# Performance work log

Hardware: AMD Instinct MI355X
Metric: run time of the kernel (lower is better)

## Reference

```python
import jax, jax.numpy as jnp
import numpy as np

N0, N1, N2 = 400000, 75000, 15000
E1, E2 = 1200000, 240000
F_IN, NC = 64, 40
H1, C1 = 2, 8          # layer 1: heads=2, out_channels=8 -> concat dim 16
H2, C2 = 1, NC         # layer 2: heads=1, out_channels=num_classes
NEG_SLOPE = 0.2


def gat_conv(x_src, x_dst, src, dst, Ws, Wd, att_s, att_d, bias, heads, ch):
    """PyG GATConv on bipartite (x_src, x_dst) with remove+add self loops."""
    n_dst = x_dst.shape[0]
    hs = (x_src @ Ws).reshape(-1, heads, ch)   # [N_src, H, C]
    hd = (x_dst @ Wd).reshape(-1, heads, ch)   # [N_dst, H, C]
    a_s = (hs * att_s).sum(-1)                 # [N_src, H]
    a_d = (hd * att_d).sum(-1)                 # [N_dst, H]
    loops = jnp.arange(n_dst)
    src_all = jnp.concatenate([src, loops])
    dst_all = jnp.concatenate([dst, loops])
    # remove_self_loops: drop pre-existing i->i edges; add_self_loops: appended
    valid = jnp.concatenate([src != dst, jnp.ones(n_dst, dtype=bool)])[:, None]
    logits = jax.nn.leaky_relu(a_s[src_all] + a_d[dst_all], NEG_SLOPE)  # [E, H]
    logits = jnp.where(valid, logits, -jnp.inf)
    m = jax.ops.segment_max(logits, dst_all, num_segments=n_dst)        # [N_dst, H]
    w = jnp.where(valid, jnp.exp(logits - m[dst_all]), 0.0)
    denom = jax.ops.segment_sum(w, dst_all, num_segments=n_dst)
    alpha = w / denom[dst_all]                                          # [E, H]
    out = jax.ops.segment_sum(alpha[:, :, None] * hs[src_all], dst_all,
                              num_segments=n_dst)                       # [N_dst, H, C]
    return out.reshape(n_dst, heads * ch) + bias


def setup_inputs() -> dict:
    key = jax.random.key(0)
    ks = jax.random.split(key, 16)
    s = 0.1
    return {
        "x": jax.random.normal(ks[0], (N0, F_IN), dtype=jnp.float32),
        "e1_src": jax.random.randint(ks[1], (E1,), 0, N0),
        "e1_dst": jax.random.randint(ks[2], (E1,), 0, N1),
        "e2_src": jax.random.randint(ks[3], (E2,), 0, N1),
        "e2_dst": jax.random.randint(ks[4], (E2,), 0, N2),
        "W1s": jax.random.normal(ks[5], (F_IN, H1 * C1), dtype=jnp.float32) * s,
        "W1d": jax.random.normal(ks[6], (F_IN, H1 * C1), dtype=jnp.float32) * s,
        "att1_s": jax.random.normal(ks[7], (H1, C1), dtype=jnp.float32) * s,
        "att1_d": jax.random.normal(ks[8], (H1, C1), dtype=jnp.float32) * s,
        "b1": jnp.zeros((H1 * C1,), dtype=jnp.float32),
        "W2s": jax.random.normal(ks[9], (H1 * C1, H2 * C2), dtype=jnp.float32) * s,
        "W2d": jax.random.normal(ks[10], (H1 * C1, H2 * C2), dtype=jnp.float32) * s,
        "att2_s": jax.random.normal(ks[11], (H2, C2), dtype=jnp.float32) * s,
        "att2_d": jax.random.normal(ks[12], (H2, C2), dtype=jnp.float32) * s,
        "b2": jnp.zeros((H2 * C2,), dtype=jnp.float32),
    }


def reference(x, e1_src, e1_dst, e2_src, e2_dst,
              W1s, W1d, att1_s, att1_d, b1,
              W2s, W2d, att2_s, att2_d, b2):
    h = gat_conv(x, x[:N1], e1_src, e1_dst, W1s, W1d, att1_s, att1_d, b1, H1, C1)
    h = jax.nn.elu(h)
    o = gat_conv(h, h[:N2], e2_src, e2_dst, W2s, W2d, att2_s, att2_d, b2, H2, C2)
    return jax.nn.log_softmax(o, axis=-1)
```

## Files before the change

kernel.cpp:

```cpp
#include <hip/hip_runtime.h>
#include <hip/hip_bf16.h>

constexpr int N0 = 400000, N1 = 75000, N2 = 15000;
constexpr int E1 = 1200000, E2 = 240000;
constexpr int NC = 40;
constexpr float NEG_SLOPE = 0.2f;

constexpr int BK1 = 128;
constexpr int NB1 = (N1 + BK1 - 1) / BK1;
constexpr int CAPB1 = 2432;
constexpr int BK2 = 32;
constexpr int NB2 = (N2 + BK2 - 1) / BK2;
constexpr int CAPB2 = 704;

constexpr int TILE = 8192;
constexpr int NT1 = (E1 + TILE - 1) / TILE;
constexpr int NT2 = (E2 + TILE - 1) / TILE;
constexpr int BPJ = (N0 + 255) / 256;

using f32x4 = __attribute__((ext_vector_type(4))) float;
using s16x8 = __attribute__((ext_vector_type(8))) short;

__device__ __forceinline__ float leaky(float v) { return v > 0.f ? v : NEG_SLOPE * v; }

__device__ __forceinline__ unsigned cvtpk(float lo, float hi) {
    unsigned r;
    asm("v_cvt_pk_bf16_f32 %0, %1, %2" : "=v"(r) : "v"(lo), "v"(hi));
    return r;
}

__device__ __forceinline__ unsigned bf16pair(float lo, float hi) {
    unsigned a = __float_as_uint(lo), b = __float_as_uint(hi);
    a = (a + 0x7FFFu + ((a >> 16) & 1u)) >> 16;
    b = (b + 0x7FFFu + ((b >> 16) & 1u)) & 0xFFFF0000u;
    return a | b;
}
__device__ __forceinline__ float bfLo(unsigned w) { return __uint_as_float(w << 16); }
__device__ __forceinline__ float bfHi(unsigned w) { return __uint_as_float(w & 0xFFFF0000u); }

__global__ __launch_bounds__(256) void k1_kernel(
    const float* __restrict__ x,
    const float* __restrict__ W1s, const float* __restrict__ W1d,
    const float* __restrict__ att1s, const float* __restrict__ att1d,
    const int* __restrict__ e1s, const int* __restrict__ e1d,
    const int* __restrict__ e2s, const int* __restrict__ e2d,
    unsigned* __restrict__ rec1, float* __restrict__ a_d1,
    int* __restrict__ gcnt1, unsigned* __restrict__ bin1,
    int* __restrict__ gcnt2, unsigned* __restrict__ bin2)
{
    __shared__ int hist[NB1];
    __shared__ int gbase[NB1];

    int bid = blockIdx.x;
    const int tid = threadIdx.x;
    if (bid < NT1 + NT2) {
        const bool isL1 = bid < NT1;
        const int* es = isL1 ? e1s : e2s;
        const int* ed = isL1 ? e1d : e2d;
        const int nE = isL1 ? E1 : E2;
        const int nb = isL1 ? NB1 : NB2;
        const int cap = isL1 ? CAPB1 : CAPB2;
        const int shift = isL1 ? 7 : 5;
        const int lsh = isL1 ? 19 : 17;
        int* gc = isL1 ? gcnt1 : gcnt2;
        unsigned* gbin = isL1 ? bin1 : bin2;
        const int base = (isL1 ? bid : bid - NT1) * TILE;
        const int lim = min(TILE, nE - base);

        for (int b = tid; b < nb; b += 256) hist[b] = 0;
        __syncthreads();
        for (int i = tid; i < lim; i += 256) {
            int s = es[base + i], d = ed[base + i];
            if (s != d) atomicAdd(&hist[d >> shift], 1);
        }
        __syncthreads();
        for (int b = tid; b < nb; b += 256) {
            int c = hist[b];
            gbase[b] = (c > 0) ? atomicAdd(&gc[b], c) : 0;
            hist[b] = 0;
        }
        __syncthreads();
        for (int i = tid; i < lim; i += 256) {
            int s = es[base + i], d = ed[base + i];
            if (s != d) {
                int b = d >> shift;
                int pos = gbase[b] + atomicAdd(&hist[b], 1);
                if (pos < cap)
                    gbin[(size_t)b * cap + pos] =
                        (unsigned)s | ((unsigned)(d & ((1 << shift) - 1)) << lsh);
            }
        }
        return;
    }
    bid -= NT1 + NT2;
    const int l    = tid & 63;
    const int nd   = l & 15;
    const int kg   = l >> 4;
    const int wv   = tid >> 6;
    const int nodeBase = bid * 256;

    s16x8 bf0, bf1;
    {
        union { unsigned u[4]; s16x8 v; } t0, t1;
        #pragma unroll
        for (int q = 0; q < 4; ++q) {
            t0.u[q] = cvtpk(W1s[(8 * kg + 2 * q) * 16 + nd],
                            W1s[(8 * kg + 2 * q + 1) * 16 + nd]);
            t1.u[q] = cvtpk(W1s[(32 + 8 * kg + 2 * q) * 16 + nd],
                            W1s[(32 + 8 * kg + 2 * q + 1) * 16 + nd]);
        }
        bf0 = t0.v; bf1 = t1.v;
    }
    float att4[4];
    #pragma unroll
    for (int r = 0; r < 4; ++r) att4[r] = att1s[4 * kg + r];

    float vdh0[16], vdh1[16];
    if (nodeBase < N1) {
        #pragma unroll
        for (int m = 0; m < 2; ++m)
            #pragma unroll
            for (int j = 0; j < 8; ++j) {
                const float* wr = W1d + (size_t)(32 * m + 8 * kg + j) * 16;
                float d0 = 0.f, d1 = 0.f;
                #pragma unroll
                for (int cc = 0; cc < 8; ++cc) {
                    d0 = fmaf(wr[cc], att1d[cc], d0);
                    d1 = fmaf(wr[8 + cc], att1d[8 + cc], d1);
                }
                vdh0[m * 8 + j] = d0; vdh1[m * 8 + j] = d1;
            }
    }

    #pragma unroll 2
    for (int rnd = 0; rnd < 4; ++rnd) {
        const int base16 = nodeBase + rnd * 64 + wv * 16;
        if (base16 >= N0) break;
        const int node = base16 + nd;
        const float* xrow = x + (size_t)node * 64;
        float4 p0 = *(const float4*)(xrow + 8 * kg);
        float4 p1 = *(const float4*)(xrow + 8 * kg + 4);
        float4 p2 = *(const float4*)(xrow + 32 + 8 * kg);
        float4 p3 = *(const float4*)(xrow + 32 + 8 * kg + 4);

        union { unsigned u[4]; s16x8 v; } a0, a1;
        a0.u[0] = cvtpk(p0.x, p0.y); a0.u[1] = cvtpk(p0.z, p0.w);
        a0.u[2] = cvtpk(p1.x, p1.y); a0.u[3] = cvtpk(p1.z, p1.w);
        a1.u[0] = cvtpk(p2.x, p2.y); a1.u[1] = cvtpk(p2.z, p2.w);
        a1.u[2] = cvtpk(p3.x, p3.y); a1.u[3] = cvtpk(p3.z, p3.w);

        f32x4 acc = {0.f, 0.f, 0.f, 0.f};
        acc = __builtin_amdgcn_mfma_f32_16x16x32_bf16(bf0, a0.v, acc, 0, 0, 0);
        acc = __builtin_amdgcn_mfma_f32_16x16x32_bf16(bf1, a1.v, acc, 0, 0, 0);

        uint2 hw;
        hw.x = cvtpk(acc[0], acc[1]);
        hw.y = cvtpk(acc[2], acc[3]);
        unsigned* rp = rec1 + (size_t)node * 16;
        *(uint2*)(rp + 2 * kg) = hw;

        float p = acc[0] * att4[0];
        p = fmaf(acc[1], att4[1], p);
        p = fmaf(acc[2], att4[2], p);
        p = fmaf(acc[3], att4[3], p);
        p += __shfl_xor(p, 16, 64);
        float q = __shfl_xor(p, 32, 64);
        if (kg == 0)
            *(uint4*)(rp + 8) = make_uint4(__float_as_uint(p), __float_as_uint(q), 0u, 0u);
        else if (kg == 1)
            *(uint4*)(rp + 12) = make_uint4(0u, 0u, 0u, 0u);

        if (base16 < N1) {
            float xv8[16] = {p0.x, p0.y, p0.z, p0.w, p1.x, p1.y, p1.z, p1.w,
                             p2.x, p2.y, p2.z, p2.w, p3.x, p3.y, p3.z, p3.w};
            float d0 = 0.f, d1 = 0.f;
            #pragma unroll
            for (int j = 0; j < 16; ++j) {
                d0 = fmaf(xv8[j], vdh0[j], d0);
                d1 = fmaf(xv8[j], vdh1[j], d1);
            }
            d0 += __shfl_xor(d0, 16, 64); d0 += __shfl_xor(d0, 32, 64);
            d1 += __shfl_xor(d1, 16, 64); d1 += __shfl_xor(d1, 32, 64);
            if (kg == 0 && node < N1)
                ((float2*)a_d1)[node] = make_float2(d0, d1);
        }
    }
}

__global__ __launch_bounds__(512) void k2_kernel(
    const int* __restrict__ gcnt1, const unsigned* __restrict__ bin1,
    const unsigned* __restrict__ rec1, const float* __restrict__ a_d1,
    const float* __restrict__ b1,
    const float* __restrict__ W2s, const float* __restrict__ W2d,
    const float* __restrict__ att2s, const float* __restrict__ att2d,
    unsigned* __restrict__ rec2)
{
    __shared__ unsigned srt[CAPB1];
    __shared__ int hist[BK1], start[BK1 + 1];
    __shared__ float w2sl[640], va[16], vd[16];
    __shared__ float h1s[BK1][17];

    const int b = blockIdx.x, tid = threadIdx.x;
    const int d0 = b * BK1;
    const int nN = min(BK1, N1 - d0);
    const int ncnt = min(gcnt1[b], CAPB1);
    const unsigned* bp = bin1 + (size_t)b * CAPB1;

    for (int i = tid; i < 640; i += 512) w2sl[i] = W2s[i];
    if (tid < BK1) hist[tid] = 0;
    if (tid >= 128 && tid < 144) {
        int k = tid - 128;
        float sa = 0.f, sd = 0.f;
        for (int cc = 0; cc < 40; ++cc) {
            sa = fmaf(W2s[k * 40 + cc], att2s[cc], sa);
            sd = fmaf(W2d[k * 40 + cc], att2d[cc], sd);
        }
        va[k] = sa; vd[k] = sd;
    }
    __syncthreads();
    for (int i = tid; i < ncnt; i += 512) atomicAdd(&hist[bp[i] >> 19], 1);
    __syncthreads();
    if (tid == 0) {
        int a = 0;
        for (int k = 0; k < BK1; ++k) { start[k] = a; a += hist[k]; }
        start[BK1] = a;
    }
    __syncthreads();
    if (tid < BK1) hist[tid] = start[tid];
    __syncthreads();
    for (int i = tid; i < ncnt; i += 512) {
        unsigned p = bp[i];
        int pos = atomicAdd(&hist[p >> 19], 1);
        srt[pos] = p & 0x7FFFFu;
    }
    __syncthreads();

    const int g = tid >> 4, c = tid & 15, h = c >> 3;
    const int wbase = tid & 48;
    const int wmap = (c < 8) ? c : (8 + ((c >> 2) & 1));
    for (int n = g; n < nN; n += 32) {
        const int node = d0 + n;
        const float ad = a_d1[(size_t)node * 2 + h];
        const int st = start[n], cnt = start[n + 1] - start[n];
        unsigned rw0 = rec1[(size_t)node * 16 + wmap];
        unsigned rw1 = (cnt >= 1) ? rec1[(size_t)srt[st] * 16 + wmap] : 0u;
        unsigned rw2 = (cnt >= 2) ? rec1[(size_t)srt[st + 1] * 16 + wmap] : 0u;
        unsigned rw3 = (cnt >= 3) ? rec1[(size_t)srt[st + 2] * 16 + wmap] : 0u;
        float accv = 0.f, den = 0.f;
        for (int j = 0; j <= cnt; ++j) {
            float asv = __uint_as_float((unsigned)__shfl((int)rw0, wbase + 8 + 4 * h, 64));
            unsigned chw = (unsigned)__shfl((int)rw0, wbase + (c >> 1), 64);
            float hv = (c & 1) ? bfHi(chw) : bfLo(chw);
            float w = __expf(leaky(asv + ad));
            accv = fmaf(w, hv, accv);
            den += w;
            rw0 = rw1; rw1 = rw2; rw2 = rw3;
            rw3 = (j + 4 <= cnt) ? rec1[(size_t)srt[st + j + 3] * 16 + wmap] : 0u;
        }
        float v = accv / den + b1[c];
        h1s[n][c] = v > 0.f ? v : (__expf(v) - 1.f);
    }
    __syncthreads();
    for (int i = tid; i < nN * 24; i += 512) {
        int nn = i / 24, w = i - nn * 24;
        unsigned* rp = rec2 + (size_t)(d0 + nn) * 24;
        if (w < 20) {
            int c0 = 2 * w, c1 = c0 + 1;
            float s0 = 0.f, s1 = 0.f;
            #pragma unroll
            for (int k = 0; k < 16; ++k) {
                float hk = h1s[nn][k];
                s0 = fmaf(hk, w2sl[k * 40 + c0], s0);
                s1 = fmaf(hk, w2sl[k * 40 + c1], s1);
            }
            rp[w] = bf16pair(s0, s1);
        } else if (w < 22) {
            const float* vv = (w == 20) ? va : vd;
            float s = 0.f;
            #pragma unroll
            for (int k = 0; k < 16; ++k) s = fmaf(h1s[nn][k], vv[k], s);
            rp[w] = __float_as_uint(s);
        }
    }
}

__global__ __launch_bounds__(1024) void k3_kernel(
    const int* __restrict__ gcnt2, const unsigned* __restrict__ bin2,
    const unsigned* __restrict__ rec2, const float* __restrict__ b2,
    float* __restrict__ out)
{
    __shared__ unsigned srt[CAPB2];
    __shared__ int hist[BK2], start[BK2 + 1];

    const int b = blockIdx.x, tid = threadIdx.x;
    const int d0 = b * BK2;
    const int nN = min(BK2, N2 - d0);
    const int ncnt = min(gcnt2[b], CAPB2);
    const unsigned* bp = bin2 + (size_t)b * CAPB2;

    if (tid < BK2) hist[tid] = 0;
    __syncthreads();
    for (int i = tid; i < ncnt; i += 1024) atomicAdd(&hist[bp[i] >> 17], 1);
    __syncthreads();
    if (tid == 0) {
        int a = 0;
        for (int k = 0; k < BK2; ++k) { start[k] = a; a += hist[k]; }
        start[BK2] = a;
    }
    __syncthreads();
    if (tid < BK2) hist[tid] = start[tid];
    __syncthreads();
    for (int i = tid; i < ncnt; i += 1024) {
        unsigned p = bp[i];
        int pos = atomicAdd(&hist[p >> 17], 1);
        srt[pos] = p & 0x1FFFFu;
    }
    __syncthreads();

    const int g = tid >> 5, l = tid & 31;
    const float bb0 = (l < 20) ? b2[2 * l] : 0.f;
    const float bb1 = (l < 20) ? b2[2 * l + 1] : 0.f;
    for (int n = g; n < nN; n += 32) {
        const int node = d0 + n;
        const int st = start[n], cnt = start[n + 1] - start[n];
        unsigned rw0 = (l < 22) ? rec2[(size_t)node * 24 + l] : 0u;
        const float ad = __uint_as_float((unsigned)__shfl((int)rw0, 21, 32));
        unsigned rw1 = (cnt >= 1 && l < 21) ? rec2[(size_t)srt[st] * 24 + l] : 0u;
        unsigned rw2 = (cnt >= 2 && l < 21) ? rec2[(size_t)srt[st + 1] * 24 + l] : 0u;
        unsigned rw3 = (cnt >= 3 && l < 21) ? rec2[(size_t)srt[st + 2] * 24 + l] : 0u;
        float a0 = 0.f, a1 = 0.f, den = 0.f;
        for (int j = 0; j <= cnt; ++j) {
            float asv = __uint_as_float((unsigned)__shfl((int)rw0, 20, 32));
            float w = __expf(leaky(asv + ad));
            a0 = fmaf(w, bfLo(rw0), a0);
            a1 = fmaf(w, bfHi(rw0), a1);
            den += w;
            rw0 = rw1; rw1 = rw2; rw2 = rw3;
            rw3 = (j + 4 <= cnt && l < 21) ? rec2[(size_t)srt[st + j + 3] * 24 + l] : 0u;
        }
        float v0 = (l < 20) ? a0 / den + bb0 : -3.4e38f;
        float v1 = (l < 20) ? a1 / den + bb1 : -3.4e38f;
        float mx = fmaxf(v0, v1);
        #pragma unroll
        for (int k = 16; k >= 1; k >>= 1) mx = fmaxf(mx, __shfl_xor(mx, k, 32));
        float ex = (l < 20) ? __expf(v0 - mx) + __expf(v1 - mx) : 0.f;
        #pragma unroll
        for (int k = 16; k >= 1; k >>= 1) ex += __shfl_xor(ex, k, 32);
        float lse = mx + logf(ex);
        if (l < 20)
            ((float2*)(out + (size_t)node * 40))[l] = make_float2(v0 - lse, v1 - lse);
    }
}

extern "C" void kernel_launch(void* const* d_in, const int* in_sizes, int n_in,
                              void* d_out, int out_size, void* d_ws, size_t ws_size,
                              hipStream_t stream) {
    const float* x      = (const float*)d_in[0];
    const int*   e1_src = (const int*)d_in[1];
    const int*   e1_dst = (const int*)d_in[2];
    const int*   e2_src = (const int*)d_in[3];
    const int*   e2_dst = (const int*)d_in[4];
    const float* W1s    = (const float*)d_in[5];
    const float* W1d    = (const float*)d_in[6];
    const float* att1s  = (const float*)d_in[7];
    const float* att1d  = (const float*)d_in[8];
    const float* b1     = (const float*)d_in[9];
    const float* W2s    = (const float*)d_in[10];
    const float* W2d    = (const float*)d_in[11];
    const float* att2s  = (const float*)d_in[12];
    const float* att2d  = (const float*)d_in[13];
    const float* b2     = (const float*)d_in[14];
    float* out = (float*)d_out;

    float* wsbase = (float*)d_ws;
    size_t o = 0;
    int*      gcnt1 = (int*)(wsbase + o);      o += NB1;
    int*      gcnt2 = (int*)(wsbase + o);      o += NB2;
    const size_t zeroWords = o;
    unsigned* bin1  = (unsigned*)(wsbase + o); o += (size_t)NB1 * CAPB1;
    unsigned* bin2  = (unsigned*)(wsbase + o); o += (size_t)NB2 * CAPB2;
    unsigned* rec1  = (unsigned*)(wsbase + o); o += (size_t)N0 * 16;
    float*    a_d1  = (float*)(wsbase + o);    o += (size_t)N1 * 2;
    unsigned* rec2  = (unsigned*)(wsbase + o); o += (size_t)N1 * 24;

    hipMemsetAsync(d_ws, 0, zeroWords * sizeof(float), stream);

    k1_kernel<<<NT1 + NT2 + BPJ, 256, 0, stream>>>(
        x, W1s, W1d, att1s, att1d, e1_src, e1_dst, e2_src, e2_dst,
        rec1, a_d1, gcnt1, bin1, gcnt2, bin2);

    k2_kernel<<<NB1, 512, 0, stream>>>(gcnt1, bin1, rec1, a_d1, b1,
                                       W2s, W2d, att2s, att2d, rec2);

    k3_kernel<<<NB2, 1024, 0, stream>>>(gcnt2, bin2, rec2, b2, out);
}
```

Before: 119.7 us.

## Software-pipeline x-row loads in k1 projection and share W1d·att1d via LDS

The node-projection part of k1 now handles 512 nodes per block in 8 rounds, with a three-stage register pipeline that issues loads for rounds ahead while computing the current one. The per-thread recomputation of W1d·att1d vectors is replaced by one 64-thread computation stored in shared memory. Launch bounds request 4 blocks per CU. This aims to hide global load latency and cut register pressure, at the cost of an extra barrier and fewer blocks for the projection phase.

```diff
diff --git a/kernel.cpp b/kernel.cpp
--- a/kernel.cpp
+++ b/kernel.cpp
@@ -16,7 +16,7 @@
 constexpr int TILE = 8192;
 constexpr int NT1 = (E1 + TILE - 1) / TILE;
 constexpr int NT2 = (E2 + TILE - 1) / TILE;
-constexpr int BPJ = (N0 + 255) / 256;
+constexpr int BPJ = (N0 + 511) / 512;
 
 using f32x4 = __attribute__((ext_vector_type(4))) float;
 using s16x8 = __attribute__((ext_vector_type(8))) short;
@@ -38,7 +38,7 @@
 __device__ __forceinline__ float bfLo(unsigned w) { return __uint_as_float(w << 16); }
 __device__ __forceinline__ float bfHi(unsigned w) { return __uint_as_float(w & 0xFFFF0000u); }
 
-__global__ __launch_bounds__(256) void k1_kernel(
+__global__ __launch_bounds__(256, 4) void k1_kernel(
     const float* __restrict__ x,
     const float* __restrict__ W1s, const float* __restrict__ W1d,
     const float* __restrict__ att1s, const float* __restrict__ att1d,
@@ -50,6 +50,7 @@
 {
     __shared__ int hist[NB1];
     __shared__ int gbase[NB1];
+    __shared__ float2 vds[64];
 
     int bid = blockIdx.x;
     const int tid = threadIdx.x;
@@ -97,7 +98,22 @@
     const int nd   = l & 15;
     const int kg   = l >> 4;
     const int wv   = tid >> 6;
-    const int nodeBase = bid * 256;
+    const int nodeBase = bid * 512;
+    const bool hasN1 = nodeBase < N1;
+
+    if (hasN1) {
+        if (tid < 64) {
+            float d0 = 0.f, d1 = 0.f;
+            const float* wr = W1d + (size_t)tid * 16;
+            #pragma unroll
+            for (int cc = 0; cc < 8; ++cc) {
+                d0 = fmaf(wr[cc], att1d[cc], d0);
+                d1 = fmaf(wr[8 + cc], att1d[8 + cc], d1);
+            }
+            vds[tid] = make_float2(d0, d1);
+        }
+        __syncthreads();
+    }
 
     s16x8 bf0, bf1;
     {
@@ -115,34 +131,20 @@
     #pragma unroll
     for (int r = 0; r < 4; ++r) att4[r] = att1s[4 * kg + r];
 
-    float vdh0[16], vdh1[16];
-    if (nodeBase < N1) {
-        #pragma unroll
-        for (int m = 0; m < 2; ++m)
-            #pragma unroll
-            for (int j = 0; j < 8; ++j) {
-                const float* wr = W1d + (size_t)(32 * m + 8 * kg + j) * 16;
-                float d0 = 0.f, d1 = 0.f;
-                #pragma unroll
-                for (int cc = 0; cc < 8; ++cc) {
-                    d0 = fmaf(wr[cc], att1d[cc], d0);
-                    d1 = fmaf(wr[8 + cc], att1d[8 + cc], d1);
-                }
-                vdh0[m * 8 + j] = d0; vdh1[m * 8 + j] = d1;
-            }
-    }
-
-    #pragma unroll 2
-    for (int rnd = 0; rnd < 4; ++rnd) {
-        const int base16 = nodeBase + rnd * 64 + wv * 16;
-        if (base16 >= N0) break;
-        const int node = base16 + nd;
-        const float* xrow = x + (size_t)node * 64;
-        float4 p0 = *(const float4*)(xrow + 8 * kg);
-        float4 p1 = *(const float4*)(xrow + 8 * kg + 4);
-        float4 p2 = *(const float4*)(xrow + 32 + 8 * kg);
-        float4 p3 = *(const float4*)(xrow + 32 + 8 * kg + 4);
-
+    const int myBase = nodeBase + wv * 16 + nd;
+
+    float4 A0, A1, A2, A3, B0, B1, B2, B3, C0, C1, C2, C3;
+
+    auto LOADr = [&](int r, float4& q0, float4& q1, float4& q2, float4& q3) {
+        int n = min(myBase + r * 64, N0 - 1);
+        const float* xr_ = x + (size_t)n * 64 + 8 * kg;
+        q0 = *(const float4*)(xr_);
+        q1 = *(const float4*)(xr_ + 4);
+        q2 = *(const float4*)(xr_ + 32);
+        q3 = *(const float4*)(xr_ + 36);
+    };
+    auto COMPUTEr = [&](int r, float4& p0, float4& p1, float4& p2, float4& p3) {
+        const int node = myBase + r * 64;
         union { unsigned u[4]; s16x8 v; } a0, a1;
         a0.u[0] = cvtpk(p0.x, p0.y); a0.u[1] = cvtpk(p0.z, p0.w);
         a0.u[2] = cvtpk(p1.x, p1.y); a0.u[3] = cvtpk(p1.z, p1.w);
@@ -152,12 +154,6 @@
         f32x4 acc = {0.f, 0.f, 0.f, 0.f};
         acc = __builtin_amdgcn_mfma_f32_16x16x32_bf16(bf0, a0.v, acc, 0, 0, 0);
         acc = __builtin_amdgcn_mfma_f32_16x16x32_bf16(bf1, a1.v, acc, 0, 0, 0);
-
-        uint2 hw;
-        hw.x = cvtpk(acc[0], acc[1]);
-        hw.y = cvtpk(acc[2], acc[3]);
-        unsigned* rp = rec1 + (size_t)node * 16;
-        *(uint2*)(rp + 2 * kg) = hw;
 
         float p = acc[0] * att4[0];
         p = fmaf(acc[1], att4[1], p);
@@ -165,26 +161,51 @@
         p = fmaf(acc[3], att4[3], p);
         p += __shfl_xor(p, 16, 64);
         float q = __shfl_xor(p, 32, 64);
-        if (kg == 0)
-            *(uint4*)(rp + 8) = make_uint4(__float_as_uint(p), __float_as_uint(q), 0u, 0u);
-        else if (kg == 1)
-            *(uint4*)(rp + 12) = make_uint4(0u, 0u, 0u, 0u);
-
-        if (base16 < N1) {
+
+        if (node < N0) {
+            unsigned* rp = rec1 + (size_t)node * 16;
+            uint2 hw;
+            hw.x = cvtpk(acc[0], acc[1]);
+            hw.y = cvtpk(acc[2], acc[3]);
+            *(uint2*)(rp + 2 * kg) = hw;
+            if (kg == 0)
+                *(uint4*)(rp + 8) = make_uint4(__float_as_uint(p), __float_as_uint(q), 0u, 0u);
+            else if (kg == 1)
+                *(uint4*)(rp + 12) = make_uint4(0u, 0u, 0u, 0u);
+        }
+        if (hasN1 && node < N1) {
             float xv8[16] = {p0.x, p0.y, p0.z, p0.w, p1.x, p1.y, p1.z, p1.w,
                              p2.x, p2.y, p2.z, p2.w, p3.x, p3.y, p3.z, p3.w};
             float d0 = 0.f, d1 = 0.f;
             #pragma unroll
-            for (int j = 0; j < 16; ++j) {
-                d0 = fmaf(xv8[j], vdh0[j], d0);
-                d1 = fmaf(xv8[j], vdh1[j], d1);
+            for (int j = 0; j < 8; ++j) {
+                float2 v = vds[8 * kg + j];
+                d0 = fmaf(xv8[j], v.x, d0);
+                d1 = fmaf(xv8[j], v.y, d1);
+            }
+            #pragma unroll
+            for (int j = 0; j < 8; ++j) {
+                float2 v = vds[32 + 8 * kg + j];
+                d0 = fmaf(xv8[8 + j], v.x, d0);
+                d1 = fmaf(xv8[8 + j], v.y, d1);
             }
             d0 += __shfl_xor(d0, 16, 64); d0 += __shfl_xor(d0, 32, 64);
             d1 += __shfl_xor(d1, 16, 64); d1 += __shfl_xor(d1, 32, 64);
-            if (kg == 0 && node < N1)
+            if (kg == 0)
                 ((float2*)a_d1)[node] = make_float2(d0, d1);
         }
-    }
+    };
+
+    LOADr(0, A0, A1, A2, A3);
+    LOADr(1, B0, B1, B2, B3);
+    LOADr(2, C0, C1, C2, C3);  COMPUTEr(0, A0, A1, A2, A3);
+    LOADr(3, A0, A1, A2, A3);  COMPUTEr(1, B0, B1, B2, B3);
+    LOADr(4, B0, B1, B2, B3);  COMPUTEr(2, C0, C1, C2, C3);
+    LOADr(5, C0, C1, C2, C3);  COMPUTEr(3, A0, A1, A2, A3);
+    LOADr(6, A0, A1, A2, A3);  COMPUTEr(4, B0, B1, B2, B3);
+    LOADr(7, B0, B1, B2, B3);  COMPUTEr(5, C0, C1, C2, C3);
+    COMPUTEr(6, A0, A1, A2, A3);
+    COMPUTEr(7, B0, B1, B2, B3);
 }
 
 __global__ __launch_bounds__(512) void k2_kernel(
```

Result: no change. 120.3 us (+0.5%).
